# Kernel tuning notes

Hardware: AMD Instinct MI355X
Metric: run time of the kernel (lower is better)

The kernel has to match this reference:

```python
import jax, jax.numpy as jnp
import numpy as np

NUM_HEADS = 16
ROTARY_BASE = 10000.0


def _apply_rotary(x):
    # x: (B, S, H, D); GPT-NeoX style rotate-half over full head dim
    B, S, H, D = x.shape
    half = D // 2
    inv_freq = 1.0 / (ROTARY_BASE ** (jnp.arange(0, half, dtype=jnp.float32) / half))
    t = jnp.arange(S, dtype=jnp.float32)
    freqs = jnp.einsum('s,d->sd', t, inv_freq)          # (S, half)
    cos = jnp.cos(freqs)[None, :, None, :]               # (1, S, 1, half)
    sin = jnp.sin(freqs)[None, :, None, :]
    x1, x2 = x[..., :half], x[..., half:]
    return jnp.concatenate([x1 * cos - x2 * sin, x2 * cos + x1 * sin], axis=-1).astype(x.dtype)


def setup_inputs() -> dict:
    key = jax.random.key(0)
    k0, k1, k2 = jax.random.split(key, 3)
    B, S, E = 2, 2048, 2048
    x = jax.random.normal(k0, (B, S, E), dtype=jnp.float32)
    wqkv = jax.random.normal(k1, (3 * E, E), dtype=jnp.float32) * 0.02
    bqkv = jnp.zeros((3 * E,), dtype=jnp.float32)
    wout = jax.random.normal(k2, (E, E), dtype=jnp.float32) * 0.02
    bout = jnp.zeros((E,), dtype=jnp.float32)
    return {"x": x, "wqkv": wqkv, "bqkv": bqkv, "wout": wout, "bout": bout}


def reference(x, wqkv, bqkv, wout, bout):
    B, S, E = x.shape
    H = NUM_HEADS
    D = E // H
    # fused QKV projection: (B, S, 3, H, D)
    qkv = (jnp.einsum('bse,fe->bsf', x, wqkv) + bqkv).reshape(B, S, 3, H, D)
    q, k, v = qkv[:, :, 0], qkv[:, :, 1], qkv[:, :, 2]
    q = _apply_rotary(q)
    k = _apply_rotary(k)
    scale = 1.0 / jnp.sqrt(jnp.float32(D))
    scores = jnp.einsum('bthd,bshd->bhts', q, k) * scale  # (B, H, S, S)
    causal_mask = jnp.triu(jnp.full((S, S), -10000.0, dtype=scores.dtype), 1)
    attn = jax.nn.softmax(scores + causal_mask, axis=-1)
    ctx = jnp.einsum('bhts,bshd->bthd', attn, v).reshape(B, S, E)
    return jnp.einsum('bse,fe->bsf', ctx, wout) + bout
```

## Files before the change

### kernel.cpp

```cpp
#include <hip/hip_runtime.h>
#include <math.h>

#define BB 2
#define SS 2048
#define EE 2048
#define HH 16
#define DD 128
#define FF 6144

typedef __attribute__((ext_vector_type(8))) short short8;
typedef __attribute__((ext_vector_type(4))) float floatx4;

static __device__ __forceinline__ unsigned short f2bf(float x) {
  unsigned u = __float_as_uint(x);
  u += 0x7fffu + ((u >> 16) & 1u);
  return (unsigned short)(u >> 16);
}
static __device__ __forceinline__ float bf2f(unsigned short h) {
  return __uint_as_float((unsigned)h << 16);
}

#define GLOAD_LDS16(gp, lp)                                       \
  __builtin_amdgcn_global_load_lds(                               \
      (const __attribute__((address_space(1))) void*)(gp),        \
      (__attribute__((address_space(3))) void*)(lp), 16, 0, 0)

__global__ __launch_bounds__(256) void cast_f32_bf16(
    const float* __restrict__ in, unsigned short* __restrict__ out, int n4) {
  const int i = blockIdx.x * 256 + threadIdx.x;
  if (i >= n4) return;
  const float4 v = ((const float4*)in)[i];
  ushort4 o;
  o.x = f2bf(v.x); o.y = f2bf(v.y); o.z = f2bf(v.z); o.w = f2bf(v.w);
  ((ushort4*)out)[i] = o;
}

static __device__ __forceinline__ void store_out(float* p, float v) { *p = v; }
static __device__ __forceinline__ void store_out(unsigned short* p, float v) {
  *p = f2bf(v);
}

template <typename OutT>
__global__ __launch_bounds__(256) void gemm_bf16_mfma(
    const unsigned short* __restrict__ A, const unsigned short* __restrict__ Bt,
    const float* __restrict__ bias, OutT* __restrict__ C,
    int M, int N, int K) {
  __shared__ unsigned short As[2][128][32];
  __shared__ unsigned short Bs[2][128][32];
  const int tid = threadIdx.x;
  const int L = tid & 63;
  const int w = tid >> 6;
  const int m0 = blockIdx.y * 128;
  const int n0 = blockIdx.x * 128;

  const int i0 = w * 2;
  const int lrow = L >> 2;
  const int lcol = (L & 3) * 8;
  const size_t a_off0 = (size_t)(m0 + (i0 + 0) * 16 + lrow) * K + lcol;
  const size_t a_off1 = (size_t)(m0 + (i0 + 1) * 16 + lrow) * K + lcol;
  const size_t b_off0 = (size_t)(n0 + (i0 + 0) * 16 + lrow) * K + lcol;
  const size_t b_off1 = (size_t)(n0 + (i0 + 1) * 16 + lrow) * K + lcol;

  const int wr = (w >> 1) * 64;
  const int wc = (w & 1) * 64;
  const int lane16 = L & 15;
  const int quad = L >> 4;

  floatx4 acc[4][4] = {};

  GLOAD_LDS16(A + a_off0, &As[0][(i0 + 0) * 16][0]);
  GLOAD_LDS16(A + a_off1, &As[0][(i0 + 1) * 16][0]);
  GLOAD_LDS16(Bt + b_off0, &Bs[0][(i0 + 0) * 16][0]);
  GLOAD_LDS16(Bt + b_off1, &Bs[0][(i0 + 1) * 16][0]);

  for (int k0 = 0; k0 < K; k0 += 32) {
    const int cur = (k0 >> 5) & 1;
    __syncthreads();
    if (k0 + 32 < K) {
      const int nxt = cur ^ 1;
      GLOAD_LDS16(A + a_off0 + k0 + 32, &As[nxt][(i0 + 0) * 16][0]);
      GLOAD_LDS16(A + a_off1 + k0 + 32, &As[nxt][(i0 + 1) * 16][0]);
      GLOAD_LDS16(Bt + b_off0 + k0 + 32, &Bs[nxt][(i0 + 0) * 16][0]);
      GLOAD_LDS16(Bt + b_off1 + k0 + 32, &Bs[nxt][(i0 + 1) * 16][0]);
    }

    short8 a[4], b[4];
#pragma unroll
    for (int mi = 0; mi < 4; ++mi)
      a[mi] = *(const short8*)(&As[cur][wr + mi * 16 + lane16][quad * 8]);
#pragma unroll
    for (int ni = 0; ni < 4; ++ni)
      b[ni] = *(const short8*)(&Bs[cur][wc + ni * 16 + lane16][quad * 8]);
#pragma unroll
    for (int mi = 0; mi < 4; ++mi)
#pragma unroll
      for (int ni = 0; ni < 4; ++ni)
        acc[mi][ni] = __builtin_amdgcn_mfma_f32_16x16x32_bf16(
            a[mi], b[ni], acc[mi][ni], 0, 0, 0);
  }

#pragma unroll
  for (int ni = 0; ni < 4; ++ni) {
    const int col = n0 + wc + ni * 16 + lane16;
    const float bv = bias[col];
#pragma unroll
    for (int mi = 0; mi < 4; ++mi) {
      const int row = m0 + wr + mi * 16 + quad * 4;
#pragma unroll
      for (int r = 0; r < 4; ++r)
        store_out(&C[(size_t)(row + r) * N + col], acc[mi][ni][r] + bv);
    }
  }
}

__global__ __launch_bounds__(256) void rotary_kernel(unsigned short* __restrict__ qkv) {
  const int idx = blockIdx.x * blockDim.x + threadIdx.x;
  const int d = idx & 63;
  const int h = (idx >> 6) & (HH - 1);
  const int s = (idx >> 10) & (SS - 1);
  const int b = idx >> 21;

  const float inv_freq = powf(10000.0f, -(float)d / 64.0f);
  const float freq = (float)s * inv_freq;
  const float c = cosf(freq);
  const float sn = sinf(freq);

  const size_t base = ((size_t)b * SS + s) * FF + h * DD + d;
  unsigned short* q = qkv + base;
  unsigned short* k = qkv + base + EE;

  const float q1 = bf2f(q[0]), q2 = bf2f(q[64]);
  q[0]  = f2bf(q1 * c - q2 * sn);
  q[64] = f2bf(q2 * c + q1 * sn);
  const float k1 = bf2f(k[0]), k2 = bf2f(k[64]);
  k[0]  = f2bf(k1 * c - k2 * sn);
  k[64] = f2bf(k2 * c + k1 * sn);
}

__global__ __launch_bounds__(256) void transpose_v(
    const unsigned short* __restrict__ qkv, unsigned short* __restrict__ vt) {
  __shared__ unsigned short T[64][72];
  const int t = threadIdx.x;
  const int s0 = blockIdx.x * 64;
  const int d0 = blockIdx.y * 64;
  const int bh = blockIdx.z;
  const int b = bh >> 4, h = bh & 15;
  {
    const int r = t >> 2, c = (t & 3) * 16;
    const unsigned short* src =
        qkv + ((size_t)b * SS + s0 + r) * FF + 2 * EE + h * DD + d0 + c;
    const uint4 u0 = *(const uint4*)src;
    const uint4 u1 = *(const uint4*)(src + 8);
    *(uint4*)&T[r][c] = u0;
    *(uint4*)&T[r][c + 8] = u1;
  }
  __syncthreads();
  {
    const int rr = t >> 2, cc = (t & 3) * 16;
    unsigned short vals[16];
#pragma unroll
    for (int j = 0; j < 16; ++j) vals[j] = T[cc + j][rr];
    unsigned short* dst =
        vt + (size_t)bh * DD * SS + (size_t)(d0 + rr) * SS + s0 + cc;
    *(uint4*)dst = *(uint4*)&vals[0];
    *(uint4*)(dst + 8) = *(uint4*)&vals[8];
  }
}

#define ATQ 128
#define ATK 32
#define SPAD 40
#define NQT (SS / ATQ)

__global__ __launch_bounds__(256, 2) void attn_mfma(
    const unsigned short* __restrict__ qkv,
    const unsigned short* __restrict__ vt,
    unsigned short* __restrict__ ctx) {
  __shared__ __align__(16) unsigned short Ksh[2][ATK * DD];
  __shared__ __align__(16) unsigned short Vsh[2][DD * ATK];
  __shared__ __align__(16) unsigned short Ssh[ATQ][SPAD];

  const int tid = threadIdx.x;
  const int L = tid & 63;
  const int w = tid >> 6;
  const int lane16 = L & 15;
  const int quad = L >> 4;

  const int flat = blockIdx.x;
  const int pi = flat >> 5;
  const int bh_lin = flat & 31;
  const int b = bh_lin >> 4;
  const int h = bh_lin & 15;
  const int bh = b * HH + h;
  const float scale = 0.08838834764831845f;

  size_t koff[2], voff[2];
  int kdst[2], vdst[2];
#pragma unroll
  for (int j = 0; j < 2; ++j) {
    const int ck = j * 256 + tid;
    const int kk = ck >> 4;
    const int cgk = (ck & 15) ^ (kk & 15);
    koff[j] = ((size_t)b * SS + kk) * FF + EE + h * DD + cgk * 8;
    kdst[j] = (j * 256 + w * 64) * 8;
    const int d = ck >> 2;
    const int cgv = (ck & 3) ^ (d & 3);
    voff[j] = (size_t)bh * DD * SS + (size_t)d * SS + cgv * 8;
    vdst[j] = kdst[j];
  }

#pragma unroll 1
  for (int phase = 0; phase < 2; ++phase) {
    const int qb = phase ? pi : (NQT - 1 - pi);
    const int q0 = qb * ATQ;

    short8 qf[2][4];
#pragma unroll
    for (int mi = 0; mi < 2; ++mi) {
      const int q = q0 + w * 32 + mi * 16 + lane16;
      const unsigned short* qp =
          qkv + ((size_t)b * SS + q) * FF + h * DD + quad * 8;
#pragma unroll
      for (int dc = 0; dc < 4; ++dc)
        qf[mi][dc] = *(const short8*)(qp + dc * 32);
    }

    floatx4 acc[8][2] = {};
    float m_i[2] = {-3.0e38f, -3.0e38f};
    float l_i[2] = {0.0f, 0.0f};

    const int nkt = 4 * qb + 4;
    const int mykt = 4 * qb + w;

#pragma unroll
    for (int j = 0; j < 2; ++j) {
      GLOAD_LDS16(qkv + koff[j], &Ksh[0][kdst[j]]);
      GLOAD_LDS16(vt + voff[j], &Vsh[0][vdst[j]]);
    }

    for (int kt = 0; kt < nkt; ++kt) {
      const int cur = kt & 1;
      __syncthreads();
      if (kt + 1 < nkt) {
        const size_t ka = (size_t)(kt + 1) * ATK * FF;
        const int va = (kt + 1) * ATK;
#pragma unroll
        for (int j = 0; j < 2; ++j) {
          GLOAD_LDS16(qkv + koff[j] + ka, &Ksh[cur ^ 1][kdst[j]]);
          GLOAD_LDS16(vt + voff[j] + va, &Vsh[cur ^ 1][vdst[j]]);
        }
      }
      if (kt > mykt) continue;
      const int k0 = kt * ATK;
      const unsigned short* Kc = Ksh[cur];
      const unsigned short* Vc = Vsh[cur];

      floatx4 st[2][2] = {};
#pragma unroll
      for (int kkt = 0; kkt < 2; ++kkt) {
        const unsigned short* krow = Kc + (kkt * 16 + lane16) * 128;
#pragma unroll
        for (int dc = 0; dc < 4; ++dc) {
          const short8 kf =
              *(const short8*)(krow + ((dc * 4 + quad) ^ lane16) * 8);
#pragma unroll
          for (int mi = 0; mi < 2; ++mi)
            st[kkt][mi] = __builtin_amdgcn_mfma_f32_16x16x32_bf16(
                kf, qf[mi][dc], st[kkt][mi], 0, 0, 0);
        }
      }

      const bool needmask = (kt == mykt);
#pragma unroll
      for (int mi = 0; mi < 2; ++mi) {
        const int q_glob = q0 + w * 32 + mi * 16 + lane16;
#pragma unroll
        for (int kkt = 0; kkt < 2; ++kkt) {
          const int kkb = k0 + kkt * 16 + quad * 4;
#pragma unroll
          for (int r = 0; r < 4; ++r) {
            float v = st[kkt][mi][r] * scale;
            if (needmask && (kkb + r) > q_glob) v = -3.0e38f;
            st[kkt][mi][r] = v;
          }
        }
      }

      float alpha[2];
#pragma unroll
      for (int mi = 0; mi < 2; ++mi) {
        float tm = -3.0e38f;
#pragma unroll
        for (int kkt = 0; kkt < 2; ++kkt)
#pragma unroll
          for (int r = 0; r < 4; ++r) tm = fmaxf(tm, st[kkt][mi][r]);
        tm = fmaxf(tm, __shfl_xor(tm, 16));
        tm = fmaxf(tm, __shfl_xor(tm, 32));
        const float mn = fmaxf(m_i[mi], tm);
        alpha[mi] = __expf(m_i[mi] - mn);
        m_i[mi] = mn;

        float rs = 0.0f;
#pragma unroll
        for (int kkt = 0; kkt < 2; ++kkt)
#pragma unroll
          for (int r = 0; r < 4; ++r) {
            const float p = __expf(st[kkt][mi][r] - mn);
            st[kkt][mi][r] = p;
            rs += p;
          }
        rs += __shfl_xor(rs, 16);
        rs += __shfl_xor(rs, 32);
        l_i[mi] = l_i[mi] * alpha[mi] + rs;

#pragma unroll
        for (int kkt = 0; kkt < 2; ++kkt) {
          ushort4 pk;
          pk.x = f2bf(st[kkt][mi][0]);
          pk.y = f2bf(st[kkt][mi][1]);
          pk.z = f2bf(st[kkt][mi][2]);
          pk.w = f2bf(st[kkt][mi][3]);
          *(ushort4*)(&Ssh[w * 32 + mi * 16 + lane16][kkt * 16 + quad * 4]) =
              pk;
        }
      }

#pragma unroll
      for (int dt = 0; dt < 8; ++dt)
#pragma unroll
        for (int mi = 0; mi < 2; ++mi)
#pragma unroll
          for (int r = 0; r < 4; ++r) acc[dt][mi][r] *= alpha[mi];

      short8 pa[2];
#pragma unroll
      for (int mi = 0; mi < 2; ++mi)
        pa[mi] = *(const short8*)(&Ssh[w * 32 + mi * 16 + lane16][quad * 8]);
      const int vpos = (quad ^ (lane16 & 3)) * 8;
#pragma unroll
      for (int dt = 0; dt < 8; ++dt) {
        const short8 vf =
            *(const short8*)(Vc + (dt * 16 + lane16) * 32 + vpos);
#pragma unroll
        for (int mi = 0; mi < 2; ++mi)
          acc[dt][mi] = __builtin_amdgcn_mfma_f32_16x16x32_bf16(
              vf, pa[mi], acc[dt][mi], 0, 0, 0);
      }
    }

#pragma unroll
    for (int mi = 0; mi < 2; ++mi) {
      const float inv = 1.0f / l_i[mi];
      const int q = q0 + w * 32 + mi * 16 + lane16;
      unsigned short* op = ctx + ((size_t)b * SS + q) * EE + h * DD + quad * 4;
#pragma unroll
      for (int dt = 0; dt < 8; ++dt) {
        ushort4 o;
        o.x = f2bf(acc[dt][mi][0] * inv);
        o.y = f2bf(acc[dt][mi][1] * inv);
        o.z = f2bf(acc[dt][mi][2] * inv);
        o.w = f2bf(acc[dt][mi][3] * inv);
        *(ushort4*)(op + dt * 16) = o;
      }
    }
  }
}

extern "C" void kernel_launch(void* const* d_in, const int* in_sizes, int n_in,
                              void* d_out, int out_size, void* d_ws,
                              size_t ws_size, hipStream_t stream) {
  const float* x    = (const float*)d_in[0];
  const float* wqkv = (const float*)d_in[1];
  const float* bqkv = (const float*)d_in[2];
  const float* wout = (const float*)d_in[3];
  const float* bout = (const float*)d_in[4];
  float* out = (float*)d_out;

  unsigned short* qkvb = (unsigned short*)d_ws;
  unsigned short* xb   = qkvb + (size_t)25165824;
  unsigned short* wqb  = xb + (size_t)8388608;
  unsigned short* ctxb = wqb + (size_t)12582912;
  unsigned short* wob  = ctxb + (size_t)8388608;
  unsigned short* vtb  = wob + (size_t)4194304;

  const int M = BB * SS;

  cast_f32_bf16<<<8192, 256, 0, stream>>>(x, xb, 2097152);
  cast_f32_bf16<<<12288, 256, 0, stream>>>(wqkv, wqb, 3145728);
  cast_f32_bf16<<<4096, 256, 0, stream>>>(wout, wob, 1048576);

  {
    dim3 grid(FF / 128, M / 128);
    gemm_bf16_mfma<unsigned short><<<grid, 256, 0, stream>>>(
        xb, wqb, bqkv, qkvb, M, FF, EE);
  }
  {
    const int total = BB * SS * HH * 64;
    rotary_kernel<<<total / 256, 256, 0, stream>>>(qkvb);
  }
  {
    dim3 grid(SS / 64, DD / 64, BB * HH);
    transpose_v<<<grid, 256, 0, stream>>>(qkvb, vtb);
  }
  {
    attn_mfma<<<dim3(256), 256, 0, stream>>>(qkvb, vtb, ctxb);
  }
  {
    dim3 grid(EE / 128, M / 128);
    gemm_bf16_mfma<float><<<grid, 256, 0, stream>>>(
        ctxb, wob, bout, out, M, EE, EE);
  }
}
```

Measured before the change: 441.2 us.

## Use 256x256-tile 8-phase pipelined MFMA GEMM for QKV projection

Adds a new GEMM kernel with 256x256 output tiles, 512 threads (8 waves) and double-buffered LDS. The K-step is split into four phases that interleave global-to-LDS prefetch, LDS reads and MFMA blocks, using barriers and setprio, and blocks are remapped across XCDs. Only the QKV projection switches to this kernel, aiming for more data reuse per tile and better overlap of loads with compute. In exchange it uses 128KB of LDS and many registers per block, and it needs hand-tuned waitcnt counts to stay correct.

```diff
diff --git a/kernel.cpp b/kernel.cpp
--- a/kernel.cpp
+++ b/kernel.cpp
@@ -113,6 +113,183 @@
   }
 }
 
+template <typename OutT>
+__global__ __launch_bounds__(512, 2) void gemm256_8ph(
+    const unsigned short* __restrict__ A, const unsigned short* __restrict__ Bt,
+    const float* __restrict__ bias, OutT* __restrict__ C,
+    int M, int N, int K) {
+  __shared__ __align__(16) unsigned short As[2][16384];
+  __shared__ __align__(16) unsigned short Bs[2][16384];
+
+  const int tid = threadIdx.x;
+  const int w = tid >> 6;
+  const int L = tid & 63;
+  const int lane16 = L & 15;
+  const int quad = L >> 4;
+  const int wm = w >> 2;
+  const int wn = w & 3;
+
+  const int nbx = N >> 8;
+  const int q8 = gridDim.x >> 3;
+  const int wg = (blockIdx.x & 7) * q8 + (blockIdx.x >> 3);
+  const int bx = wg % nbx;
+  const int by = wg / nbx;
+  const int m0 = by << 8;
+  const int n0 = bx << 8;
+
+  const int lA = ((w >> 1) << 4) + (L >> 2);
+  const int scol = ((w & 1) << 5) + (((L & 3) * 8) ^ ((L & 32) ? 16 : 0));
+  unsigned aoff[4], boff[4];
+#pragma unroll
+  for (int j = 0; j < 4; ++j) {
+    const int ra = ((j & 1) << 7) | ((j >> 1) << 6) | lA;
+    aoff[j] = (unsigned)(m0 + ra) * (unsigned)K + scol;
+    const int lB = j * 64 + lA;
+    const int rB = (((lB >> 5) & 3) << 6) | (((lB >> 7) & 1) << 5) | (lB & 31);
+    boff[j] = (unsigned)(n0 + rB) * (unsigned)K + scol;
+  }
+  const int ldst = w * 512;
+
+  const int sq = (quad * 8) ^ ((lane16 & 8) << 1);
+  const int rbase = lane16 * 32 + sq;
+
+  floatx4 acc[8][4] = {};
+
+  GLOAD_LDS16(A + aoff[0], &As[0][0 * 4096 + ldst]);
+  GLOAD_LDS16(A + aoff[1], &As[0][1 * 4096 + ldst]);
+  GLOAD_LDS16(Bt + boff[0], &Bs[0][0 * 4096 + ldst]);
+  GLOAD_LDS16(Bt + boff[1], &Bs[0][1 * 4096 + ldst]);
+  GLOAD_LDS16(Bt + boff[2], &Bs[0][2 * 4096 + ldst]);
+  GLOAD_LDS16(Bt + boff[3], &Bs[0][3 * 4096 + ldst]);
+  GLOAD_LDS16(A + aoff[2], &As[0][2 * 4096 + ldst]);
+  GLOAD_LDS16(A + aoff[3], &As[0][3 * 4096 + ldst]);
+  asm volatile("s_waitcnt vmcnt(4)" ::: "memory");
+  __builtin_amdgcn_s_barrier();
+
+  const int NT = K >> 6;
+  short8 a[4][2], b0[2][2], b1[2][2];
+
+  for (int t = 0; t < NT; ++t) {
+    const int c = t & 1;
+    const int nc = c ^ 1;
+    const unsigned kn = (unsigned)(t + 1) << 6;
+    const bool pf = (t + 1 < NT);
+    const unsigned short* Ac = &As[c][0];
+    const unsigned short* Bc = &Bs[c][0];
+
+#pragma unroll
+    for (int i = 0; i < 4; ++i)
+#pragma unroll
+      for (int kk = 0; kk < 2; ++kk)
+        a[i][kk] = *(const short8*)(Ac + ((wm * 4 + i) * 2 + kk) * 512 + rbase);
+#pragma unroll
+    for (int j = 0; j < 2; ++j)
+#pragma unroll
+      for (int kk = 0; kk < 2; ++kk)
+        b0[j][kk] = *(const short8*)(Bc + ((wn * 2 + j) * 2 + kk) * 512 + rbase);
+    if (pf) {
+      GLOAD_LDS16(A + aoff[0] + kn, &As[nc][0 * 4096 + ldst]);
+      GLOAD_LDS16(A + aoff[1] + kn, &As[nc][1 * 4096 + ldst]);
+    }
+    asm volatile("s_waitcnt lgkmcnt(8)" ::: "memory");
+    __builtin_amdgcn_s_barrier();
+    asm volatile("s_waitcnt lgkmcnt(0)" ::: "memory");
+    __builtin_amdgcn_s_setprio(1);
+#pragma unroll
+    for (int i = 0; i < 4; ++i)
+#pragma unroll
+      for (int j = 0; j < 2; ++j)
+#pragma unroll
+        for (int kk = 0; kk < 2; ++kk)
+          acc[i][j] = __builtin_amdgcn_mfma_f32_16x16x32_bf16(
+              a[i][kk], b0[j][kk], acc[i][j], 0, 0, 0);
+    __builtin_amdgcn_s_setprio(0);
+    asm volatile("s_waitcnt vmcnt(4)" ::: "memory");
+    __builtin_amdgcn_s_barrier();
+
+#pragma unroll
+    for (int j = 0; j < 2; ++j)
+#pragma unroll
+      for (int kk = 0; kk < 2; ++kk)
+        b1[j][kk] =
+            *(const short8*)(Bc + ((8 + wn * 2 + j) * 2 + kk) * 512 + rbase);
+    if (pf) {
+      GLOAD_LDS16(Bt + boff[0] + kn, &Bs[nc][0 * 4096 + ldst]);
+      GLOAD_LDS16(Bt + boff[1] + kn, &Bs[nc][1 * 4096 + ldst]);
+    }
+    __builtin_amdgcn_s_barrier();
+    asm volatile("s_waitcnt lgkmcnt(0)" ::: "memory");
+    __builtin_amdgcn_s_setprio(1);
+#pragma unroll
+    for (int i = 0; i < 4; ++i)
+#pragma unroll
+      for (int j = 0; j < 2; ++j)
+#pragma unroll
+        for (int kk = 0; kk < 2; ++kk)
+          acc[i][2 + j] = __builtin_amdgcn_mfma_f32_16x16x32_bf16(
+              a[i][kk], b1[j][kk], acc[i][2 + j], 0, 0, 0);
+    __builtin_amdgcn_s_setprio(0);
+    asm volatile("s_waitcnt vmcnt(4)" ::: "memory");
+    __builtin_amdgcn_s_barrier();
+
+#pragma unroll
+    for (int i = 0; i < 4; ++i)
+#pragma unroll
+      for (int kk = 0; kk < 2; ++kk)
+        a[i][kk] =
+            *(const short8*)(Ac + ((8 + wm * 4 + i) * 2 + kk) * 512 + rbase);
+    if (pf) {
+      GLOAD_LDS16(Bt + boff[2] + kn, &Bs[nc][2 * 4096 + ldst]);
+      GLOAD_LDS16(Bt + boff[3] + kn, &Bs[nc][3 * 4096 + ldst]);
+    }
+    __builtin_amdgcn_s_barrier();
+    asm volatile("s_waitcnt lgkmcnt(0)" ::: "memory");
+    __builtin_amdgcn_s_setprio(1);
+#pragma unroll
+    for (int i = 0; i < 4; ++i)
+#pragma unroll
+      for (int j = 0; j < 2; ++j)
+#pragma unroll
+        for (int kk = 0; kk < 2; ++kk)
+          acc[4 + i][2 + j] = __builtin_amdgcn_mfma_f32_16x16x32_bf16(
+              a[i][kk], b1[j][kk], acc[4 + i][2 + j], 0, 0, 0);
+    __builtin_amdgcn_s_setprio(0);
+    asm volatile("s_waitcnt vmcnt(4)" ::: "memory");
+    __builtin_amdgcn_s_barrier();
+
+    if (pf) {
+      GLOAD_LDS16(A + aoff[2] + kn, &As[nc][2 * 4096 + ldst]);
+      GLOAD_LDS16(A + aoff[3] + kn, &As[nc][3 * 4096 + ldst]);
+    }
+    __builtin_amdgcn_s_barrier();
+    __builtin_amdgcn_s_setprio(1);
+#pragma unroll
+    for (int i = 0; i < 4; ++i)
+#pragma unroll
+      for (int j = 0; j < 2; ++j)
+#pragma unroll
+        for (int kk = 0; kk < 2; ++kk)
+          acc[4 + i][j] = __builtin_amdgcn_mfma_f32_16x16x32_bf16(
+              a[i][kk], b0[j][kk], acc[4 + i][j], 0, 0, 0);
+    __builtin_amdgcn_s_setprio(0);
+    asm volatile("s_waitcnt vmcnt(4)" ::: "memory");
+    __builtin_amdgcn_s_barrier();
+  }
+
+#pragma unroll
+  for (int ni = 0; ni < 4; ++ni) {
+    const int col = n0 + wn * 64 + ni * 16 + lane16;
+    const float bv = bias[col];
+#pragma unroll
+    for (int mi = 0; mi < 8; ++mi) {
+      const int row = m0 + wm * 128 + mi * 16 + quad * 4;
+#pragma unroll
+      for (int r = 0; r < 4; ++r)
+        store_out(&C[(size_t)(row + r) * N + col], acc[mi][ni][r] + bv);
+    }
+  }
+}
+
 __global__ __launch_bounds__(256) void rotary_kernel(unsigned short* __restrict__ qkv) {
   const int idx = blockIdx.x * blockDim.x + threadIdx.x;
   const int d = idx & 63;
@@ -390,8 +567,7 @@
   cast_f32_bf16<<<4096, 256, 0, stream>>>(wout, wob, 1048576);
 
   {
-    dim3 grid(FF / 128, M / 128);
-    gemm_bf16_mfma<unsigned short><<<grid, 256, 0, stream>>>(
+    gemm256_8ph<unsigned short><<<dim3(384), 512, 0, stream>>>(
         xb, wqb, bqkv, qkvb, M, FF, EE);
   }
   {
```

Result: slower. 452.9 us (+2.7%).
